# Kernel tuning notes

Hardware: AMD Instinct MI355X
Metric: run time of the kernel (lower is better)

Reference implementation:

```python
import jax, jax.numpy as jnp
import numpy as np

B, T = 32, 64
C, H, W = 1, 32, 32
A, E, D, S, HID = 2, 64, 128, 32, 128
K, STRIDE, PAD = 4, 2, 1
FEAT = 64 * 4 * 4  # conv stack output: 64 channels at 4x4


def _lin(x, w, b):
    return x @ w.T + b


def _conv(x, w, b):
    y = jax.lax.conv_general_dilated(x, w, (STRIDE, STRIDE), [(PAD, PAD)] * 2,
                                     dimension_numbers=('NCHW', 'OIHW', 'NCHW'))
    return y + b[None, :, None, None]


def _deconv(x, w, b):
    # torch ConvTranspose2d(w: (in_c,out_c,k,k), stride=2, pad=1) as dilated conv
    w_ = jnp.flip(w, (2, 3)).transpose(1, 0, 2, 3)
    p = K - 1 - PAD
    y = jax.lax.conv_general_dilated(x, w_, (1, 1), [(p, p)] * 2,
                                     lhs_dilation=(STRIDE, STRIDE),
                                     dimension_numbers=('NCHW', 'OIHW', 'NCHW'))
    return y + b[None, :, None, None]


def _mlp(x, w1, b1, w2, b2, w3, b3):
    h = jax.nn.elu(_lin(x, w1, b1))
    h = jax.nn.elu(_lin(h, w2, b2))
    out = _lin(h, w3, b3)
    return out[..., :S], jnp.clip(out[..., S:], -5.0, 2.0)


def _gru(x, h, wih, whh, bih, bhh):
    # torch nn.GRUCell semantics
    gi = x @ wih.T + bih
    gh = h @ whh.T + bhh
    ir, iz, inn = jnp.split(gi, 3, -1)
    hr, hz, hn = jnp.split(gh, 3, -1)
    r = jax.nn.sigmoid(ir + hr)
    u = jax.nn.sigmoid(iz + hz)
    n = jnp.tanh(inn + r * hn)
    return (1.0 - u) * n + u * h


def setup_inputs():
    keys = iter(jax.random.split(jax.random.key(0), 64))

    def p(shape, fan):
        return jax.random.normal(next(keys), shape, jnp.float32) / np.sqrt(fan)

    return dict(
        obs=jax.random.normal(next(keys), (B, T, C, H, W), jnp.float32),
        actions=jax.random.normal(next(keys), (B, T, A), jnp.float32),
        noise=jax.random.normal(next(keys), (T, B, S), jnp.float32),
        enc_w1=p((32, C, K, K), C * K * K), enc_b1=jnp.zeros(32),
        enc_w2=p((64, 32, K, K), 32 * K * K), enc_b2=jnp.zeros(64),
        enc_w3=p((64, 64, K, K), 64 * K * K), enc_b3=jnp.zeros(64),
        enc_pw=p((E, FEAT), FEAT), enc_pb=jnp.zeros(E),
        dec_pw=p((FEAT, D + S), D + S), dec_pb=jnp.zeros(FEAT),
        dec_w1=p((64, 64, K, K), 64 * K * K), dec_b1=jnp.zeros(64),
        dec_w2=p((64, 32, K, K), 64 * K * K), dec_b2=jnp.zeros(32),
        dec_w3=p((32, C, K, K), 32 * K * K), dec_b3=jnp.zeros(C),
        gru_wih=p((3 * D, S + A), D), gru_whh=p((3 * D, D), D),
        gru_bih=jnp.zeros(3 * D), gru_bhh=jnp.zeros(3 * D),
        pri_w1=p((HID, D + A), D + A), pri_b1=jnp.zeros(HID),
        pri_w2=p((HID, HID), HID), pri_b2=jnp.zeros(HID),
        pri_w3=p((2 * S, HID), HID), pri_b3=jnp.zeros(2 * S),
        pos_w1=p((HID, D + E), D + E), pos_b1=jnp.zeros(HID),
        pos_w2=p((HID, HID), HID), pos_b2=jnp.zeros(HID),
        pos_w3=p((2 * S, HID), HID), pos_b3=jnp.zeros(2 * S),
    )


def reference(obs, actions, noise, enc_w1, enc_b1, enc_w2, enc_b2, enc_w3, enc_b3,
              enc_pw, enc_pb, dec_pw, dec_pb, dec_w1, dec_b1, dec_w2, dec_b2,
              dec_w3, dec_b3, gru_wih, gru_whh, gru_bih, gru_bhh,
              pri_w1, pri_b1, pri_w2, pri_b2, pri_w3, pri_b3,
              pos_w1, pos_b1, pos_w2, pos_b2, pos_w3, pos_b3):
    Bq, Tq = obs.shape[:2]
    # --- CNN encoder over all frames at once ---
    x = obs.reshape(Bq * Tq, C, H, W)
    x = jax.nn.relu(_conv(x, enc_w1, enc_b1))
    x = jax.nn.relu(_conv(x, enc_w2, enc_b2))
    x = jax.nn.relu(_conv(x, enc_w3, enc_b3))
    embed = _lin(x.reshape(Bq * Tq, -1), enc_pw, enc_pb).reshape(Bq, Tq, E)

    # --- sequential RSSM core (use_posterior=True path) ---
    def step(h, inp):
        a, e_t, eps = inp
        pm, pls = _mlp(jnp.concatenate([h, e_t], -1),
                       pos_w1, pos_b1, pos_w2, pos_b2, pos_w3, pos_b3)
        z = pm + jnp.exp(pls) * eps
        prm, prls = _mlp(jnp.concatenate([h, a], -1),
                         pri_w1, pri_b1, pri_w2, pri_b2, pri_w3, pri_b3)
        h_new = _gru(jnp.concatenate([z, a], -1), h, gru_wih, gru_whh, gru_bih, gru_bhh)
        return h_new, (z, prm, prls, pm, pls, h)  # h = pre-update (used for decode)

    h0 = jnp.zeros((Bq, D), obs.dtype)
    h_final, (zs, prm, prls, pm, pls, hs) = jax.lax.scan(
        step, h0, (actions.swapaxes(0, 1), embed.swapaxes(0, 1), noise))

    # --- batched decode of all (h_t, z_t); same math as per-step decode ---
    hz = jnp.concatenate([hs, zs], -1).reshape(Tq * Bq, D + S)
    y = _lin(hz, dec_pw, dec_pb).reshape(Tq * Bq, 64, 4, 4)
    y = jax.nn.relu(_deconv(y, dec_w1, dec_b1))
    y = jax.nn.relu(_deconv(y, dec_w2, dec_b2))
    y = jax.nn.sigmoid(_deconv(y, dec_w3, dec_b3))
    recons = y.reshape(Tq, Bq, C, H, W).swapaxes(0, 1)

    tb = lambda t: t.swapaxes(0, 1)  # (T,B,.) -> (B,T,.)
    return (recons, tb(zs), tb(prm), tb(prls), tb(pm), tb(pls), h_final)
```

## Files before the change

### kernel.cpp

```cpp
#include <hip/hip_runtime.h>
#include <math.h>

#define NB 32
#define NT 64
#define NF 2048

#define OUT_ZS    2097152
#define OUT_PRM   (OUT_ZS + 65536)
#define OUT_PRLS  (OUT_PRM + 65536)
#define OUT_PM    (OUT_PRLS + 65536)
#define OUT_PLS   (OUT_PM + 65536)
#define OUT_HF    (OUT_PLS + 65536)

#define WS_HS    27394048
#define WS_ENCT  27656192
#define WS_WP1H  27885568
#define WS_WP2   27893760
#define WS_WP3   27901952
#define WS_WWHH  27906048
#define WS_WIHZ  27930624
#define WS_PW1T  27977984
#define WS_WIHT  28002560
#define WS_WC2   16777216
#define WS_WC3   (WS_WC2 + 16384)
#define WS_WD1   (WS_WC3 + 32768)
#define WS_WD2   (WS_WD1 + 32768)
#define WS_DLIN  16908288
#define WS_DECWF 17960960
#define WS_QW1F  18045952
#define WS_QW2F  18057216
#define WS_QW3F  18066432
#define WS_POSL1E 25165824
#define WS_GIA    (WS_POSL1E + 262144)

typedef __attribute__((ext_vector_type(8))) short short8;
typedef __attribute__((ext_vector_type(4))) float floatx4;
typedef _Float16 __attribute__((ext_vector_type(2))) half2v;
typedef _Float16 __attribute__((ext_vector_type(8))) half8;
union U4S8 { uint4 u; short8 s; };
__device__ __forceinline__ short8 u2s(uint4 u) { U4S8 x; x.u = u; return x.s; }
union U4HH { uint4 u; half8 h; };
__device__ __forceinline__ half8 u2hh(uint4 u) { U4HH x; x.u = u; return x.h; }

__device__ __forceinline__ float rcpf(float x) {
#if __has_builtin(__builtin_amdgcn_rcpf)
  return __builtin_amdgcn_rcpf(x);
#else
  return 1.f / x;
#endif
}
__device__ __forceinline__ float eluf(float a) {
  return (a > 0.f) ? a : (__expf(a) - 1.f);
}
__device__ __forceinline__ float sigm(float a) {
  return rcpf(1.f + __expf(-a));
}
__device__ __forceinline__ float tanhfast(float x) {
  const float e = __expf(fminf(-2.f * x, 60.f));
  return (1.f - e) * rcpf(1.f + e);
}
__device__ __forceinline__ unsigned short f2bf(float f) {
  unsigned int u = __float_as_uint(f);
  u += 0x7fffu + ((u >> 16) & 1u);
  return (unsigned short)(u >> 16);
}
__device__ __forceinline__ unsigned short f2h(float f) {
  _Float16 h = (_Float16)f;
  return __builtin_bit_cast(unsigned short, h);
}
__device__ __forceinline__ unsigned int pack2h(float a, float b) {
  return (unsigned int)f2h(a) | ((unsigned int)f2h(b) << 16);
}
union UH2 { unsigned int u; half2v h; };
__device__ __forceinline__ half2v u2h(unsigned int u) { UH2 x; x.u = u; return x.h; }

__device__ __forceinline__ float fdot2w(half2v a, half2v b, float c) {
#if __has_builtin(__builtin_amdgcn_fdot2)
  return __builtin_amdgcn_fdot2(a, b, c, false);
#else
  return fmaf((float)a[0], (float)b[0], fmaf((float)a[1], (float)b[1], c));
#endif
}

union U4H2 { uint4 u; half2v h[4]; };
__device__ __forceinline__ void dot8h(uint4 w, uint4 x,
                                      float& a0, float& a1, float& a2, float& a3) {
  U4H2 W; W.u = w;
  U4H2 X; X.u = x;
  a0 = fdot2w(W.h[0], X.h[0], a0);
  a1 = fdot2w(W.h[1], X.h[1], a1);
  a2 = fdot2w(W.h[2], X.h[2], a2);
  a3 = fdot2w(W.h[3], X.h[3], a3);
}

struct PP { const float* src; void* dst; int n; int mode; int A; int B; };
struct PPAll { PP m[16]; };

__global__ __launch_bounds__(256) void k_prep(PPAll a) {
  PP p = a.m[blockIdx.y];
  for (int i = blockIdx.x * 256 + threadIdx.x; i < p.n; i += gridDim.x * 256) {
    if (p.mode == 10) {
      const int r = i / p.B, c = i - r * p.B;
      ((float*)p.dst)[c * p.A + r] = p.src[i];
    } else {
      float v;
      if (p.mode == 0) v = p.src[i];
      else if (p.mode == 1) v = p.src[(i >> 7) * 192 + (i & 127)];
      else if (p.mode == 2) v = p.src[(i >> 5) * 34 + (i & 31)];
      else if (p.mode == 6) {
        const int o = i / 160, k = i - o * 160;
        v = (k < 130) ? p.src[o * 130 + k] : 0.f;
      } else {
        const int ab = p.A * p.B;
        const int t = i / ab, rem = i - t * ab;
        const int oc = rem / p.B, ic = rem - oc * p.B;
        v = (p.mode == 3) ? p.src[(oc * p.B + ic) * 16 + t]
                          : p.src[(ic * p.A + oc) * 16 + t];
      }
      ((unsigned short*)p.dst)[i] = (p.mode <= 2 || p.mode == 6) ? f2h(v) : f2bf(v);
    }
  }
}

__global__ __launch_bounds__(256, 3) void k_enc(
    const float* __restrict__ obs, const float* __restrict__ act,
    const float* __restrict__ w1, const float* __restrict__ b1,
    const unsigned short* __restrict__ wc2, const float* __restrict__ b2,
    const unsigned short* __restrict__ wc3, const float* __restrict__ b3,
    const float* __restrict__ encT, const float* __restrict__ encb,
    const float* __restrict__ pw1T, const float* __restrict__ pb1,
    const float* __restrict__ wihT, const float* __restrict__ bih,
    const float* __restrict__ bhh,
    float* __restrict__ posl1e, float* __restrict__ gia) {
  const int f = blockIdx.x, tid = threadIdx.x;
  const int w = tid >> 6, l = tid & 63, q = l >> 4, n = l & 15;
  __shared__ float sIn1[32 * 33];
  __shared__ float sW1[512];
  __shared__ float sB1[32];
  __shared__ __align__(16) unsigned short sIn2[18 * 18 * 40];
  __shared__ __align__(16) unsigned short sIn3[10 * 10 * 72];
  __shared__ __align__(16) float sXe[1024];
  __shared__ float sP[256];
  __shared__ float sE[64];
  __shared__ float sA2[2];

  {
    const float* in = obs + (size_t)f * 1024;
    for (int i = tid; i < 1024; i += 256) sIn1[(i >> 5) * 33 + (i & 31)] = in[i];
    for (int i = tid; i < 512; i += 256) sW1[i] = w1[i];
    if (tid < 32) sB1[tid] = b1[tid];
    if (tid < 2) sA2[tid] = act[(size_t)f * 2 + tid];
    unsigned int* z2 = (unsigned int*)sIn2;
    for (int i = tid; i < 18 * 18 * 40 / 2; i += 256) z2[i] = 0u;
    unsigned int* z3 = (unsigned int*)sIn3;
    for (int i = tid; i < 10 * 10 * 72 / 2; i += 256) z3[i] = 0u;
  }
  __syncthreads();
  for (int r = tid; r < 512; r += 256) {
    const int oc = r >> 4, oy = r & 15;
    float acc[16];
    const float bv = sB1[oc];
#pragma unroll
    for (int j = 0; j < 16; j++) acc[j] = bv;
#pragma unroll
    for (int ky = 0; ky < 4; ky++) {
      const int iy = 2 * oy + ky - 1;
      if (iy < 0 || iy >= 32) continue;
#pragma unroll
      for (int kx = 0; kx < 4; kx++) {
        const float wv = sW1[oc * 16 + ky * 4 + kx];
#pragma unroll
        for (int j = 0; j < 16; j++) {
          const int ix = 2 * j + kx - 1;
          if (ix >= 0 && ix < 32) acc[j] += wv * sIn1[iy * 33 + ix];
        }
      }
    }
#pragma unroll
    for (int j = 0; j < 16; j++)
      sIn2[((oy + 1) * 18 + (j + 1)) * 40 + oc] = f2bf(fmaxf(acc[j], 0.f));
  }
  __syncthreads();
  {
    int base[4];
#pragma unroll
    for (int nt = 0; nt < 4; nt++) {
      const int px = nt * 16 + n, oy = px >> 3, ox = px & 7;
      base[nt] = ((2 * oy + 1) * 18 + (2 * ox + 1)) * 40 + q * 8;
    }
    floatx4 acc[4];
#pragma unroll
    for (int nt = 0; nt < 4; nt++) acc[nt] = (floatx4){0.f, 0.f, 0.f, 0.f};
    uint4 af[16];
#pragma unroll
    for (int t = 0; t < 16; t++)
      af[t] = *reinterpret_cast<const uint4*>(wc2 + (size_t)(t * 64 + w * 16 + n) * 32 + q * 8);
#pragma unroll
    for (int t = 0; t < 16; t++) {
      const int toff = ((t / 4 - 1) * 18 + (t % 4 - 1)) * 40;
#pragma unroll
      for (int nt = 0; nt < 4; nt++) {
        uint4 bf = *reinterpret_cast<const uint4*>(&sIn2[base[nt] + toff]);
        acc[nt] = __builtin_amdgcn_mfma_f32_16x16x32_bf16(u2s(af[t]), u2s(bf), acc[nt], 0, 0, 0);
      }
    }
    float b4[4];
#pragma unroll
    for (int r = 0; r < 4; r++) b4[r] = b2[w * 16 + q * 4 + r];
    __syncthreads();
#pragma unroll
    for (int nt = 0; nt < 4; nt++) {
      const int px = nt * 16 + n, oy = px >> 3, ox = px & 7;
#pragma unroll
      for (int r = 0; r < 4; r++)
        sIn3[((oy + 1) * 10 + (ox + 1)) * 72 + (w * 16 + q * 4 + r)] =
            f2bf(fmaxf(acc[nt][r] + b4[r], 0.f));
    }
  }
  __syncthreads();
  {
    const int oy = n >> 2, ox = n & 3;
    const int ibase = ((2 * oy + 1) * 10 + (2 * ox + 1)) * 72 + q * 8;
    floatx4 acc = (floatx4){0.f, 0.f, 0.f, 0.f};
    for (int ks = 0; ks < 2; ks++) {
      uint4 af[16];
#pragma unroll
      for (int t = 0; t < 16; t++)
        af[t] = *reinterpret_cast<const uint4*>(
            wc3 + (size_t)(t * 64 + w * 16 + n) * 64 + ks * 32 + q * 8);
#pragma unroll
      for (int t = 0; t < 16; t++) {
        const int toff = ((t / 4 - 1) * 10 + (t % 4 - 1)) * 72 + ks * 32;
        uint4 bf = *reinterpret_cast<const uint4*>(&sIn3[ibase + toff]);
        acc = __builtin_amdgcn_mfma_f32_16x16x32_bf16(u2s(af[t]), u2s(bf), acc, 0, 0, 0);
      }
    }
#pragma unroll
    for (int r = 0; r < 4; r++) {
      const int ch = w * 16 + q * 4 + r;
      sXe[ch * 16 + n] = fmaxf(acc[r] + b3[ch], 0.f);
    }
  }
  __syncthreads();
  {
    const int o = tid & 63, s = tid >> 6;
    float acc = 0.f;
    const int k0 = s * 256;
    for (int k = k0; k < k0 + 256; k++) acc += encT[k * 64 + o] * sXe[k];
    sP[tid] = acc;
  }
  __syncthreads();
  if (tid < 64)
    sE[tid] = sP[tid] + sP[tid + 64] + sP[tid + 128] + sP[tid + 192] + encb[tid];
  __syncthreads();
  if (tid < 128) {
    float a = pb1[tid];
    for (int k = 0; k < 64; k++) a += pw1T[(128 + k) * 128 + tid] * sE[k];
    posl1e[(size_t)f * 128 + tid] = a;
  } else {
#pragma unroll
    for (int jj = 0; jj < 3; jj++) {
      const int j = (tid - 128) + jj * 128;
      gia[(size_t)f * 384 + (tid - 128) * 3 + jj] =
          bih[j] + bhh[j] + wihT[32 * 384 + j] * sA2[0] + wihT[33 * 384 + j] * sA2[1];
    }
  }
}

__global__ __launch_bounds__(512, 2) void k_rssm4(
    const float* __restrict__ posl1e, const float* __restrict__ gia,
    const float* __restrict__ noise,
    const unsigned short* __restrict__ wp1h, const unsigned short* __restrict__ wp2,
    const unsigned short* __restrict__ wp3, const unsigned short* __restrict__ wwhh,
    const unsigned short* __restrict__ wihz,
    const float* __restrict__ pb2, const float* __restrict__ pb3,
    float* __restrict__ hs, float* __restrict__ out) {
  const int b = blockIdx.x, tid = threadIdx.x;
  const int R = tid >> 2, ks4 = tid & 3;
  __shared__ __align__(16) _Float16 sHh[128];
  __shared__ __align__(16) _Float16 sL1h[128];
  __shared__ __align__(16) _Float16 sL2h[128];
  __shared__ __align__(16) _Float16 sZh[32];
  __shared__ float sGh[384];

  uint4 wA4[4][4];
  {
#pragma unroll
    for (int j = 0; j < 4; j++) {
      const unsigned short* p = (j == 0)
          ? (wp1h + R * 128)
          : (wwhh + (size_t)((j - 1) * 128 + R) * 128);
      const uint4* pv = reinterpret_cast<const uint4*>(p + ks4 * 32);
#pragma unroll
      for (int i = 0; i < 4; i++) wA4[j][i] = pv[i];
    }
  }
  uint4 wB[4];
  {
    const unsigned short* rowB = wp2 + R * 128 + ks4 * 32;
#pragma unroll
    for (int i = 0; i < 4; i++) wB[i] = reinterpret_cast<const uint4*>(rowB)[i];
  }
  uint4 wC[2];
  {
    const int r = tid >> 3;
    const int o = (r >> 1) + ((r & 1) << 5);
    const unsigned short* rowC = wp3 + o * 128 + (tid & 7) * 16;
#pragma unroll
    for (int i = 0; i < 2; i++) wC[i] = reinterpret_cast<const uint4*>(rowC)[i];
  }
  uint4 wD[3][4];
  if (tid < 128) {
#pragma unroll
    for (int j = 0; j < 3; j++) {
      const unsigned short* rowD = wihz + (size_t)(tid + 128 * j) * 32;
#pragma unroll
      for (int i = 0; i < 4; i++) wD[j][i] = reinterpret_cast<const uint4*>(rowD)[i];
    }
  }
  const bool zlane = (tid & 15) == 0;
  const int jz = tid >> 4;
  const float pb2R = pb2[R];
  const float pb3mR = zlane ? pb3[jz] : 0.f;
  const float pb3sR = zlane ? pb3[jz + 32] : 0.f;

  float h_reg = 0.f;
  float pl1R = 0.f, epsR = 0.f;
  float3 gaR = {0.f, 0.f, 0.f};
  if (ks4 == 0) pl1R = posl1e[(size_t)(b * 64) * 128 + R];
  if (tid < 128) {
    gaR = *reinterpret_cast<const float3*>(&gia[(size_t)(b * 64) * 384 + tid * 3]);
    sHh[tid] = (_Float16)0.f;
    hs[(size_t)b * 128 + tid] = 0.f;
  }
  if (zlane) epsR = noise[(size_t)b * 32 + jz];
  __syncthreads();

  for (int t = 0; t < 64; ++t) {
    const int tn = (t < 63) ? t + 1 : 63;
    float pl1N = 0.f, epsN = 0.f;
    float3 gaN = {0.f, 0.f, 0.f};
    if (ks4 == 0) pl1N = posl1e[(size_t)(b * 64 + tn) * 128 + R];
    if (tid < 128)
      gaN = *reinterpret_cast<const float3*>(&gia[(size_t)(b * 64 + tn) * 384 + tid * 3]);
    if (zlane) epsN = noise[(size_t)(tn * 32 + b) * 32 + jz];

    {
      const uint4* xs = reinterpret_cast<const uint4*>(sHh) + ks4 * 4;
      const uint4 x0 = xs[0], x1 = xs[1], x2 = xs[2], x3 = xs[3];
      float part[4];
#pragma unroll
      for (int j = 0; j < 4; j++) {
        float p0 = 0.f, p1 = 0.f, p2 = 0.f, p3 = 0.f;
        dot8h(wA4[j][0], x0, p0, p1, p2, p3);
        dot8h(wA4[j][1], x1, p0, p1, p2, p3);
        dot8h(wA4[j][2], x2, p0, p1, p2, p3);
        dot8h(wA4[j][3], x3, p0, p1, p2, p3);
        part[j] = (p0 + p1) + (p2 + p3);
      }
#pragma unroll
      for (int j = 0; j < 4; j++) {
        part[j] += __shfl_xor(part[j], 1);
        part[j] += __shfl_xor(part[j], 2);
      }
      if (ks4 == 0) {
        sL1h[R] = (_Float16)eluf(part[0] + pl1R);
        sGh[R * 3] = part[1];
        sGh[R * 3 + 1] = part[2];
        sGh[R * 3 + 2] = part[3];
      }
    }
    __syncthreads();
    {
      float a0 = 0.f, a1 = 0.f, a2 = 0.f, a3 = 0.f;
      const uint4* xs = reinterpret_cast<const uint4*>(sL1h) + ks4 * 4;
#pragma unroll
      for (int i = 0; i < 4; i++) dot8h(wB[i], xs[i], a0, a1, a2, a3);
      float p = (a0 + a1) + (a2 + a3);
      p += __shfl_xor(p, 1);
      p += __shfl_xor(p, 2);
      if (ks4 == 0) sL2h[R] = (_Float16)eluf(p + pb2R);
    }
    __syncthreads();
    {
      float a0 = 0.f, a1 = 0.f, a2 = 0.f, a3 = 0.f;
      const uint4* xs = reinterpret_cast<const uint4*>(sL2h) + (tid & 7) * 2;
      dot8h(wC[0], xs[0], a0, a1, a2, a3);
      dot8h(wC[1], xs[1], a0, a1, a2, a3);
      float p = (a0 + a1) + (a2 + a3);
      p += __shfl_xor(p, 1);
      p += __shfl_xor(p, 2);
      p += __shfl_xor(p, 4);
      const float pq = __shfl_xor(p, 8);
      if (zlane) {
        const float pm = p + pb3mR;
        float pls = pq + pb3sR;
        pls = fminf(fmaxf(pls, -5.f), 2.f);
        const float z = pm + __expf(pls) * epsR;
        sZh[jz] = (_Float16)z;
        const int o = (b * 64 + t) * 32 + jz;
        out[OUT_ZS + o] = z;
        out[OUT_PM + o] = pm;
        out[OUT_PLS + o] = pls;
      }
    }
    __syncthreads();
    if (tid < 128) {
      float r0 = 0.f, r1 = 0.f, r2 = 0.f, r3 = 0.f;
      float u0 = 0.f, u1 = 0.f, u2 = 0.f, u3 = 0.f;
      float m0 = 0.f, m1 = 0.f, m2 = 0.f, m3 = 0.f;
      const uint4* xs = reinterpret_cast<const uint4*>(sZh);
#pragma unroll
      for (int i = 0; i < 4; i++) {
        const uint4 xv = xs[i];
        dot8h(wD[0][i], xv, r0, r1, r2, r3);
        dot8h(wD[1][i], xv, u0, u1, u2, u3);
        dot8h(wD[2][i], xv, m0, m1, m2, m3);
      }
      const float gr = gaR.x + ((r0 + r1) + (r2 + r3));
      const float gu = gaR.y + ((u0 + u1) + (u2 + u3));
      const float gn = gaR.z + ((m0 + m1) + (m2 + m3));
      const float ghr = sGh[tid * 3];
      const float ghu = sGh[tid * 3 + 1];
      const float ghn = sGh[tid * 3 + 2];
      const float r = sigm(gr + ghr);
      const float u = sigm(gu + ghu);
      const float n = tanhfast(gn + r * ghn);
      const float hn = (1.f - u) * n + u * h_reg;
      h_reg = hn;
      sHh[tid] = (_Float16)hn;
      if (t < 63) hs[(size_t)((t + 1) * 32 + b) * 128 + tid] = hn;
    }
    pl1R = pl1N;
    gaR = gaN;
    epsR = epsN;
    __syncthreads();
  }
  if (tid < 128) out[OUT_HF + b * 128 + tid] = h_reg;
}

__global__ __launch_bounds__(256) void k_post(
    const float* __restrict__ hs, const float* __restrict__ zs,
    const unsigned short* __restrict__ decwf, const float* __restrict__ decb,
    unsigned short* __restrict__ dlin,
    const float* __restrict__ act,
    const unsigned short* __restrict__ qw1f, const float* __restrict__ qb1,
    const unsigned short* __restrict__ qw2f, const float* __restrict__ qb2,
    const unsigned short* __restrict__ qw3f, const float* __restrict__ qb3,
    float* __restrict__ out) {
  const int tid = threadIdx.x;
  const int bid = blockIdx.x;
  const int w = tid >> 6, l = tid & 63, q = l >> 4, n = l & 15;
  __shared__ __align__(16) _Float16 sB[16][168];
  __shared__ __align__(16) _Float16 sB2[16][136];

  if (bid < 2048) {
    const int otile = bid & 15;
    const int fBase = (bid >> 4) * 16;
    for (int i = tid; i < 2560; i += 256) {
      const int fr = i / 160, k = i - fr * 160;
      const int f = fBase + fr;
      float v;
      if (k < 128) v = hs[(size_t)f * 128 + k];
      else v = zs[(size_t)((f & 31) * 64 + (f >> 5)) * 32 + (k - 128)];
      sB[fr][k] = (_Float16)v;
    }
    __syncthreads();
    const int oB = otile * 64 + w * 16;
    floatx4 acc = (floatx4){0.f, 0.f, 0.f, 0.f};
#pragma unroll
    for (int ks = 0; ks < 5; ks++) {
      uint4 a = *reinterpret_cast<const uint4*>(&decwf[(size_t)(oB + n) * 160 + ks * 32 + q * 8]);
      uint4 bb = *reinterpret_cast<const uint4*>(&sB[n][ks * 32 + q * 8]);
      acc = __builtin_amdgcn_mfma_f32_16x16x32_f16(u2hh(a), u2hh(bb), acc, 0, 0, 0);
    }
    const int o0 = oB + q * 4;
    const int f = fBase + n;
    const unsigned int lo = (unsigned int)f2bf(acc[0] + decb[o0]) |
                            ((unsigned int)f2bf(acc[1] + decb[o0 + 1]) << 16);
    const unsigned int hi = (unsigned int)f2bf(acc[2] + decb[o0 + 2]) |
                            ((unsigned int)f2bf(acc[3] + decb[o0 + 3]) << 16);
    *reinterpret_cast<uint2*>(&dlin[(size_t)f * 1024 + o0]) = make_uint2(lo, hi);
    return;
  }
  const int fBase = (bid - 2048) * 16;
  for (int i = tid; i < 2560; i += 256) {
    const int fr = i / 160, k = i - fr * 160;
    const int f = fBase + fr;
    float v = 0.f;
    if (k < 128) v = hs[(size_t)f * 128 + k];
    else if (k < 130) v = act[(size_t)((f & 31) * 64 + (f >> 5)) * 2 + (k - 128)];
    sB[fr][k] = (_Float16)v;
  }
  __syncthreads();
#pragma unroll
  for (int g = 0; g < 2; g++) {
    const int oB = g * 64 + w * 16;
    floatx4 acc = (floatx4){0.f, 0.f, 0.f, 0.f};
#pragma unroll
    for (int ks = 0; ks < 5; ks++) {
      uint4 a = *reinterpret_cast<const uint4*>(&qw1f[(oB + n) * 160 + ks * 32 + q * 8]);
      uint4 bb = *reinterpret_cast<const uint4*>(&sB[n][ks * 32 + q * 8]);
      acc = __builtin_amdgcn_mfma_f32_16x16x32_f16(u2hh(a), u2hh(bb), acc, 0, 0, 0);
    }
    const int o0 = oB + q * 4;
    *reinterpret_cast<unsigned int*>(&sB2[n][o0]) =
        pack2h(eluf(acc[0] + qb1[o0]), eluf(acc[1] + qb1[o0 + 1]));
    *reinterpret_cast<unsigned int*>(&sB2[n][o0 + 2]) =
        pack2h(eluf(acc[2] + qb1[o0 + 2]), eluf(acc[3] + qb1[o0 + 3]));
  }
  __syncthreads();
#pragma unroll
  for (int g = 0; g < 2; g++) {
    const int oB = g * 64 + w * 16;
    floatx4 acc = (floatx4){0.f, 0.f, 0.f, 0.f};
#pragma unroll
    for (int ks = 0; ks < 4; ks++) {
      uint4 a = *reinterpret_cast<const uint4*>(&qw2f[(oB + n) * 128 + ks * 32 + q * 8]);
      uint4 bb = *reinterpret_cast<const uint4*>(&sB2[n][ks * 32 + q * 8]);
      acc = __builtin_amdgcn_mfma_f32_16x16x32_f16(u2hh(a), u2hh(bb), acc, 0, 0, 0);
    }
    const int o0 = oB + q * 4;
    *reinterpret_cast<unsigned int*>(&sB[n][o0]) =
        pack2h(eluf(acc[0] + qb2[o0]), eluf(acc[1] + qb2[o0 + 1]));
    *reinterpret_cast<unsigned int*>(&sB[n][o0 + 2]) =
        pack2h(eluf(acc[2] + qb2[o0 + 2]), eluf(acc[3] + qb2[o0 + 3]));
  }
  __syncthreads();
  {
    const int oB = w * 16;
    floatx4 acc = (floatx4){0.f, 0.f, 0.f, 0.f};
#pragma unroll
    for (int ks = 0; ks < 4; ks++) {
      uint4 a = *reinterpret_cast<const uint4*>(&qw3f[(oB + n) * 128 + ks * 32 + q * 8]);
      uint4 bb = *reinterpret_cast<const uint4*>(&sB[n][ks * 32 + q * 8]);
      acc = __builtin_amdgcn_mfma_f32_16x16x32_f16(u2hh(a), u2hh(bb), acc, 0, 0, 0);
    }
    const int o0 = oB + q * 4;
    const int f = fBase + n;
    const int ob = ((f & 31) * 64 + (f >> 5)) * 32;
#pragma unroll
    for (int r = 0; r < 4; r++) {
      const int o = o0 + r;
      const float v = acc[r] + qb3[o];
      if (o < 32) out[OUT_PRM + ob + o] = v;
      else out[OUT_PRLS + ob + o - 32] = fminf(fmaxf(v, -5.f), 2.f);
    }
  }
}

#define D3_ROW 580
#define D3_PX  36
__global__ __launch_bounds__(256, 4) void k_dec(
    const unsigned short* __restrict__ dlin,
    const unsigned short* __restrict__ wd1, const float* __restrict__ db1,
    const unsigned short* __restrict__ wd2, const float* __restrict__ db2,
    const float* __restrict__ w3, const float* __restrict__ b3,
    float* __restrict__ out) {
  const int f = blockIdx.x, tid = threadIdx.x;
  const int w = tid >> 6, l = tid & 63, q = l >> 4, n = l & 15;
  const int t = f >> 5, b = f & 31;
  __shared__ __align__(16) unsigned short sInD1[6 * 6 * 72];
  __shared__ __align__(16) unsigned short sInD2[10 * 10 * 72];
  __shared__ __align__(16) _Float16 sInD3h[16 * D3_ROW];
  __shared__ __align__(16) _Float16 sW3h[16 * 32];

  const uint2 dv = *reinterpret_cast<const uint2*>(dlin + (size_t)f * 1024 + tid * 4);
  {
    unsigned int* z1 = (unsigned int*)sInD1;
    for (int i = tid; i < 6 * 6 * 72 / 2; i += 256) z1[i] = 0u;
    unsigned int* z2 = (unsigned int*)sInD2;
    for (int i = tid; i < 10 * 10 * 72 / 2; i += 256) z2[i] = 0u;
    for (int s = tid; s < 512; s += 256) {
      const int tap = s >> 5, icc = s & 31;
      sW3h[s] = (_Float16)w3[icc * 16 + tap];
    }
  }
  __syncthreads();
  {
    const int o0 = tid * 4, c = o0 >> 4, px0 = o0 & 15;
    const int Y = px0 >> 2;
    const int base = ((Y + 1) * 6 + 1) * 72 + c;
    sInD1[base] = (unsigned short)(dv.x & 0xffffu);
    sInD1[base + 72] = (unsigned short)(dv.x >> 16);
    sInD1[base + 144] = (unsigned short)(dv.y & 0xffffu);
    sInD1[base + 216] = (unsigned short)(dv.y >> 16);
  }
  __syncthreads();
  {
    const int Y = n >> 2, X = n & 3;
    const int ibase = ((Y + 1) * 6 + (X + 1)) * 72 + q * 8;
    float b4[4];
#pragma unroll
    for (int r = 0; r < 4; r++) b4[r] = db1[w * 16 + q * 4 + r];
#pragma unroll
    for (int c = 0; c < 4; c++) {
      const int cy = c >> 1, cx = c & 1;
      floatx4 acc = (floatx4){0.f, 0.f, 0.f, 0.f};
      for (int ks = 0; ks < 2; ks++) {
        uint4 af[4];
#pragma unroll
        for (int tt = 0; tt < 4; tt++) {
          const int t2 = tt >> 1, t3 = tt & 1;
          const int ky = ((cy + 1) & 1) + 2 * t2, kx = ((cx + 1) & 1) + 2 * t3;
          af[tt] = *reinterpret_cast<const uint4*>(
              wd1 + (size_t)((ky * 4 + kx) * 64 + w * 16 + n) * 64 + ks * 32 + q * 8);
        }
#pragma unroll
        for (int tt = 0; tt < 4; tt++) {
          const int t2 = tt >> 1, t3 = tt & 1;
          const int toff = ((cy - t2) * 6 + (cx - t3)) * 72 + ks * 32;
          uint4 bf = *reinterpret_cast<const uint4*>(&sInD1[ibase + toff]);
          acc = __builtin_amdgcn_mfma_f32_16x16x32_bf16(u2s(af[tt]), u2s(bf), acc, 0, 0, 0);
        }
      }
      const int oy = 2 * Y + cy, ox = 2 * X + cx;
#pragma unroll
      for (int r = 0; r < 4; r++)
        sInD2[((oy + 1) * 10 + (ox + 1)) * 72 + (w * 16 + q * 4 + r)] =
            f2bf(fmaxf(acc[r] + b4[r], 0.f));
    }
  }
  __syncthreads();
  {
    const int px = w * 16 + n;
    const int Y = px >> 3, X = px & 7;
    const int ibase = ((Y + 1) * 10 + (X + 1)) * 72 + q * 8;
    float b4[2][4];
#pragma unroll
    for (int mi = 0; mi < 2; mi++)
#pragma unroll
      for (int r = 0; r < 4; r++) b4[mi][r] = db2[mi * 16 + q * 4 + r];
#pragma unroll
    for (int c = 0; c < 4; c++) {
      const int cy = c >> 1, cx = c & 1;
      floatx4 acc[2];
      acc[0] = (floatx4){0.f, 0.f, 0.f, 0.f};
      acc[1] = (floatx4){0.f, 0.f, 0.f, 0.f};
      for (int ks = 0; ks < 2; ks++) {
        uint4 af[2][4];
#pragma unroll
        for (int mi = 0; mi < 2; mi++)
#pragma unroll
          for (int tt = 0; tt < 4; tt++) {
            const int t2 = tt >> 1, t3 = tt & 1;
            const int ky = ((cy + 1) & 1) + 2 * t2, kx = ((cx + 1) & 1) + 2 * t3;
            af[mi][tt] = *reinterpret_cast<const uint4*>(
                wd2 + (size_t)((ky * 4 + kx) * 32 + mi * 16 + n) * 64 + ks * 32 + q * 8);
          }
#pragma unroll
        for (int tt = 0; tt < 4; tt++) {
          const int t2 = tt >> 1, t3 = tt & 1;
          const int toff = ((cy - t2) * 10 + (cx - t3)) * 72 + ks * 32;
          uint4 bf = *reinterpret_cast<const uint4*>(&sInD2[ibase + toff]);
#pragma unroll
          for (int mi = 0; mi < 2; mi++)
            acc[mi] = __builtin_amdgcn_mfma_f32_16x16x32_bf16(u2s(af[mi][tt]), u2s(bf),
                                                              acc[mi], 0, 0, 0);
        }
      }
      const int oy = 2 * Y + cy, ox = 2 * X + cx;
#pragma unroll
      for (int mi = 0; mi < 2; mi++) {
        const unsigned int lo =
            (unsigned int)f2h(fmaxf(acc[mi][0] + b4[mi][0], 0.f)) |
            ((unsigned int)f2h(fmaxf(acc[mi][1] + b4[mi][1], 0.f)) << 16);
        const unsigned int hi =
            (unsigned int)f2h(fmaxf(acc[mi][2] + b4[mi][2], 0.f)) |
            ((unsigned int)f2h(fmaxf(acc[mi][3] + b4[mi][3], 0.f)) << 16);
        *reinterpret_cast<uint2*>(&sInD3h[oy * D3_ROW + ox * D3_PX + mi * 16 + q * 4]) =
            make_uint2(lo, hi);
      }
    }
  }
  __syncthreads();
  {
    const int oy = tid >> 3;
    const int rem2 = tid & 7;
    const int cpar = rem2 >> 2, qq = rem2 & 3;
    const int py = (oy + 1) & 1, pc = (cpar + 1) & 1;
    const int ixb0 = (cpar + 1 - pc) >> 1;
    const int xlo = ixb0 - 1 + qq * 4;
    float acc[4] = {0.f, 0.f, 0.f, 0.f};
    const float bv = b3[0];
#pragma unroll
    for (int u2 = 0; u2 < 2; u2++) {
      const int ky = py + 2 * u2;
      const int iy = (oy + 1 - ky) >> 1;
      if (iy < 0 || iy >= 16) continue;
      const _Float16* rowp = &sInD3h[iy * D3_ROW];
      const uint2* wAp = reinterpret_cast<const uint2*>(&sW3h[(ky * 4 + pc) * 32]);
      const uint2* wBp = reinterpret_cast<const uint2*>(&sW3h[(ky * 4 + pc + 2) * 32]);
#pragma unroll
      for (int kb = 0; kb < 8; kb++) {
        uint2 xv[5];
#pragma unroll
        for (int x = 0; x < 5; x++) {
          const int ix = xlo + x;
          xv[x] = (ix >= 0 && ix < 16)
              ? *reinterpret_cast<const uint2*>(&rowp[ix * D3_PX + kb * 4])
              : make_uint2(0u, 0u);
        }
        const uint2 wa = wAp[kb], wb = wBp[kb];
#pragma unroll
        for (int j = 0; j < 4; j++) {
          acc[j] = fdot2w(u2h(wa.x), u2h(xv[j + 1].x), acc[j]);
          acc[j] = fdot2w(u2h(wa.y), u2h(xv[j + 1].y), acc[j]);
          acc[j] = fdot2w(u2h(wb.x), u2h(xv[j].x), acc[j]);
          acc[j] = fdot2w(u2h(wb.y), u2h(xv[j].y), acc[j]);
        }
      }
    }
    const int fo = b * 64 + t;
    float* yf = out + (size_t)fo * 1024;
#pragma unroll
    for (int j = 0; j < 4; j++)
      yf[oy * 32 + (cpar + 2 * (qq * 4 + j))] = rcpf(1.f + __expf(-(acc[j] + bv)));
  }
}

extern "C" void kernel_launch(void* const* d_in, const int* in_sizes, int n_in,
                              void* d_out, int out_size, void* d_ws, size_t ws_size,
                              hipStream_t stream) {
  const float* obs = (const float*)d_in[0];
  const float* actions = (const float*)d_in[1];
  const float* noise = (const float*)d_in[2];
  const float* enc_w1 = (const float*)d_in[3];
  const float* enc_b1 = (const float*)d_in[4];
  const float* enc_w2 = (const float*)d_in[5];
  const float* enc_b2 = (const float*)d_in[6];
  const float* enc_w3 = (const float*)d_in[7];
  const float* enc_b3 = (const float*)d_in[8];
  const float* enc_pw = (const float*)d_in[9];
  const float* enc_pb = (const float*)d_in[10];
  const float* dec_pw = (const float*)d_in[11];
  const float* dec_pb = (const float*)d_in[12];
  const float* dec_w1 = (const float*)d_in[13];
  const float* dec_b1 = (const float*)d_in[14];
  const float* dec_w2 = (const float*)d_in[15];
  const float* dec_b2 = (const float*)d_in[16];
  const float* dec_w3 = (const float*)d_in[17];
  const float* dec_b3 = (const float*)d_in[18];
  const float* gru_wih = (const float*)d_in[19];
  const float* gru_whh = (const float*)d_in[20];
  const float* gru_bih = (const float*)d_in[21];
  const float* gru_bhh = (const float*)d_in[22];
  const float* pri_w1 = (const float*)d_in[23];
  const float* pri_b1 = (const float*)d_in[24];
  const float* pri_w2 = (const float*)d_in[25];
  const float* pri_b2 = (const float*)d_in[26];
  const float* pri_w3 = (const float*)d_in[27];
  const float* pri_b3 = (const float*)d_in[28];
  const float* pos_w1 = (const float*)d_in[29];
  const float* pos_b1 = (const float*)d_in[30];
  const float* pos_w2 = (const float*)d_in[31];
  const float* pos_b2 = (const float*)d_in[32];
  const float* pos_w3 = (const float*)d_in[33];
  const float* pos_b3 = (const float*)d_in[34];

  float* out = (float*)d_out;
  float* ws = (float*)d_ws;
  float* HS = ws + WS_HS;
  float* POSL1E = ws + WS_POSL1E;
  float* GIA = ws + WS_GIA;
  unsigned short* WP1H = (unsigned short*)(ws + WS_WP1H);
  unsigned short* WP2 = (unsigned short*)(ws + WS_WP2);
  unsigned short* WP3 = (unsigned short*)(ws + WS_WP3);
  unsigned short* WWHH = (unsigned short*)(ws + WS_WWHH);
  unsigned short* WIHZ = (unsigned short*)(ws + WS_WIHZ);
  unsigned short* WC2 = (unsigned short*)(ws + WS_WC2);
  unsigned short* WC3 = (unsigned short*)(ws + WS_WC3);
  unsigned short* WD1 = (unsigned short*)(ws + WS_WD1);
  unsigned short* WD2 = (unsigned short*)(ws + WS_WD2);
  unsigned short* DLIN = (unsigned short*)(ws + WS_DLIN);
  unsigned short* DECWF = (unsigned short*)(ws + WS_DECWF);
  unsigned short* QW1F = (unsigned short*)(ws + WS_QW1F);
  unsigned short* QW2F = (unsigned short*)(ws + WS_QW2F);
  unsigned short* QW3F = (unsigned short*)(ws + WS_QW3F);

  PPAll pp;
  pp.m[0]  = {enc_pw, ws + WS_ENCT, 64 * 1024, 10, 64, 1024};
  pp.m[1]  = {dec_pw, DECWF, 1024 * 160, 0, 0, 0};
  pp.m[2]  = {pri_w1, QW1F, 128 * 160, 6, 0, 0};
  pp.m[3]  = {pri_w2, QW2F, 128 * 128, 0, 0, 0};
  pp.m[4]  = {pri_w3, QW3F, 64 * 128, 0, 0, 0};
  pp.m[5]  = {pos_w1, ws + WS_PW1T, 128 * 192, 10, 128, 192};
  pp.m[6]  = {gru_wih, ws + WS_WIHT, 384 * 34, 10, 384, 34};
  pp.m[7]  = {pos_w1, WP1H, 128 * 128, 1, 0, 0};
  pp.m[8]  = {pos_w2, WP2, 128 * 128, 0, 0, 0};
  pp.m[9]  = {pos_w3, WP3, 64 * 128, 0, 0, 0};
  pp.m[10] = {gru_whh, WWHH, 384 * 128, 0, 0, 0};
  pp.m[11] = {gru_wih, WIHZ, 384 * 32, 2, 0, 0};
  pp.m[12] = {enc_w2, WC2, 16 * 64 * 32, 3, 64, 32};
  pp.m[13] = {enc_w3, WC3, 16 * 64 * 64, 3, 64, 64};
  pp.m[14] = {dec_w1, WD1, 16 * 64 * 64, 4, 64, 64};
  pp.m[15] = {dec_w2, WD2, 16 * 32 * 64, 4, 32, 64};
  hipLaunchKernelGGL(k_prep, dim3(32, 16), dim3(256), 0, stream, pp);

  k_enc<<<NF, 256, 0, stream>>>(obs, actions, enc_w1, enc_b1, WC2, enc_b2,
                                WC3, enc_b3, ws + WS_ENCT, enc_pb,
                                ws + WS_PW1T, pos_b1, ws + WS_WIHT, gru_bih,
                                gru_bhh, POSL1E, GIA);

  k_rssm4<<<NB, 512, 0, stream>>>(POSL1E, GIA, noise, WP1H, WP2, WP3, WWHH, WIHZ,
                                  pos_b2, pos_b3, HS, out);

  k_post<<<2176, 256, 0, stream>>>(HS, out + OUT_ZS, DECWF, dec_pb, DLIN,
                                   actions, QW1F, pri_b1, QW2F, pri_b2,
                                   QW3F, pri_b3, out);

  k_dec<<<NF, 256, 0, stream>>>(DLIN, WD1, dec_b1, WD2, dec_b2, dec_w3, dec_b3, out);
}
```

Before: 437.8 us.

## Move encoder projection and posterior layer-1 embed term to batched MFMA kernel

The per-frame scalar GEMV for the encoder projection (1024->64) and the posterior first-layer embedding contribution are removed from k_enc. k_enc now writes fp16 conv features to workspace, and a new k_emb kernel processes 16 frames per block with f16 MFMA, using fp16 copies of the weights prepared in k_prep. The aim is to replace slow per-frame fp32 dot products with tensor-core GEMMs that reuse the weights across frames. The cost is an extra launch and a global round trip for the features, plus reduced precision from fp16 rounding of the features and the embedding.

```diff
diff --git a/kernel.cpp b/kernel.cpp
--- a/kernel.cpp
+++ b/kernel.cpp
@@ -13,13 +13,13 @@
 #define OUT_HF    (OUT_PLS + 65536)
 
 #define WS_HS    27394048
-#define WS_ENCT  27656192
+#define WS_ENCWF 27656192
 #define WS_WP1H  27885568
 #define WS_WP2   27893760
 #define WS_WP3   27901952
 #define WS_WWHH  27906048
 #define WS_WIHZ  27930624
-#define WS_PW1T  27977984
+#define WS_PW1E  27977984
 #define WS_WIHT  28002560
 #define WS_WC2   16777216
 #define WS_WC3   (WS_WC2 + 16384)
@@ -30,6 +30,7 @@
 #define WS_QW1F  18045952
 #define WS_QW2F  18057216
 #define WS_QW3F  18066432
+#define WS_XE    18874368
 #define WS_POSL1E 25165824
 #define WS_GIA    (WS_POSL1E + 262144)
 
@@ -110,6 +111,8 @@
       else if (p.mode == 6) {
         const int o = i / 160, k = i - o * 160;
         v = (k < 130) ? p.src[o * 130 + k] : 0.f;
+      } else if (p.mode == 7) {
+        v = p.src[(i >> 6) * 192 + 128 + (i & 63)];
       } else {
         const int ab = p.A * p.B;
         const int t = i / ab, rem = i - t * ab;
@@ -117,7 +120,7 @@
         v = (p.mode == 3) ? p.src[(oc * p.B + ic) * 16 + t]
                           : p.src[(ic * p.A + oc) * 16 + t];
       }
-      ((unsigned short*)p.dst)[i] = (p.mode <= 2 || p.mode == 6) ? f2h(v) : f2bf(v);
+      ((unsigned short*)p.dst)[i] = (p.mode <= 2 || p.mode >= 6) ? f2h(v) : f2bf(v);
     }
   }
 }
@@ -127,11 +130,9 @@
     const float* __restrict__ w1, const float* __restrict__ b1,
     const unsigned short* __restrict__ wc2, const float* __restrict__ b2,
     const unsigned short* __restrict__ wc3, const float* __restrict__ b3,
-    const float* __restrict__ encT, const float* __restrict__ encb,
-    const float* __restrict__ pw1T, const float* __restrict__ pb1,
     const float* __restrict__ wihT, const float* __restrict__ bih,
     const float* __restrict__ bhh,
-    float* __restrict__ posl1e, float* __restrict__ gia) {
+    unsigned short* __restrict__ xe, float* __restrict__ gia) {
   const int f = blockIdx.x, tid = threadIdx.x;
   const int w = tid >> 6, l = tid & 63, q = l >> 4, n = l & 15;
   __shared__ float sIn1[32 * 33];
@@ -139,9 +140,7 @@
   __shared__ float sB1[32];
   __shared__ __align__(16) unsigned short sIn2[18 * 18 * 40];
   __shared__ __align__(16) unsigned short sIn3[10 * 10 * 72];
-  __shared__ __align__(16) float sXe[1024];
-  __shared__ float sP[256];
-  __shared__ float sE[64];
+  __shared__ __align__(16) _Float16 sXeh[1024];
   __shared__ float sA2[2];
 
   {
@@ -238,32 +237,71 @@
 #pragma unroll
     for (int r = 0; r < 4; r++) {
       const int ch = w * 16 + q * 4 + r;
-      sXe[ch * 16 + n] = fmaxf(acc[r] + b3[ch], 0.f);
-    }
-  }
-  __syncthreads();
-  {
-    const int o = tid & 63, s = tid >> 6;
-    float acc = 0.f;
-    const int k0 = s * 256;
-    for (int k = k0; k < k0 + 256; k++) acc += encT[k * 64 + o] * sXe[k];
-    sP[tid] = acc;
-  }
-  __syncthreads();
-  if (tid < 64)
-    sE[tid] = sP[tid] + sP[tid + 64] + sP[tid + 128] + sP[tid + 192] + encb[tid];
-  __syncthreads();
-  if (tid < 128) {
-    float a = pb1[tid];
-    for (int k = 0; k < 64; k++) a += pw1T[(128 + k) * 128 + tid] * sE[k];
-    posl1e[(size_t)f * 128 + tid] = a;
-  } else {
+      sXeh[ch * 16 + n] = (_Float16)fmaxf(acc[r] + b3[ch], 0.f);
+    }
+  }
+  __syncthreads();
+  *reinterpret_cast<uint2*>(&xe[(size_t)f * 1024 + tid * 4]) =
+      *reinterpret_cast<const uint2*>(&sXeh[tid * 4]);
+  if (tid >= 128) {
 #pragma unroll
     for (int jj = 0; jj < 3; jj++) {
       const int j = (tid - 128) + jj * 128;
       gia[(size_t)f * 384 + (tid - 128) * 3 + jj] =
           bih[j] + bhh[j] + wihT[32 * 384 + j] * sA2[0] + wihT[33 * 384 + j] * sA2[1];
     }
+  }
+}
+
+__global__ __launch_bounds__(256) void k_emb(
+    const unsigned short* __restrict__ xe,
+    const unsigned short* __restrict__ encwf, const float* __restrict__ encb,
+    const unsigned short* __restrict__ pw1e, const float* __restrict__ pb1,
+    float* __restrict__ posl1e) {
+  const int tid = threadIdx.x;
+  const int fBase = blockIdx.x * 16;
+  const int w = tid >> 6, l = tid & 63, q = l >> 4, n = l & 15;
+  __shared__ __align__(16) _Float16 sB[16][1032];
+  __shared__ __align__(16) _Float16 sE2[16][72];
+#pragma unroll
+  for (int j = 0; j < 8; j++) {
+    const int i4 = tid + j * 256;
+    const int fr = i4 >> 7, kq = (i4 & 127) * 8;
+    *reinterpret_cast<uint4*>(&sB[fr][kq]) =
+        *reinterpret_cast<const uint4*>(&xe[(size_t)(fBase + fr) * 1024 + kq]);
+  }
+  __syncthreads();
+  {
+    const int oB = w * 16;
+    floatx4 acc = (floatx4){0.f, 0.f, 0.f, 0.f};
+#pragma unroll
+    for (int ks = 0; ks < 32; ks++) {
+      uint4 a = *reinterpret_cast<const uint4*>(
+          &encwf[(size_t)(oB + n) * 1024 + ks * 32 + q * 8]);
+      uint4 bb = *reinterpret_cast<const uint4*>(&sB[n][ks * 32 + q * 8]);
+      acc = __builtin_amdgcn_mfma_f32_16x16x32_f16(u2hh(a), u2hh(bb), acc, 0, 0, 0);
+    }
+    const int o0 = oB + q * 4;
+    *reinterpret_cast<unsigned int*>(&sE2[n][o0]) =
+        pack2h(acc[0] + encb[o0], acc[1] + encb[o0 + 1]);
+    *reinterpret_cast<unsigned int*>(&sE2[n][o0 + 2]) =
+        pack2h(acc[2] + encb[o0 + 2], acc[3] + encb[o0 + 3]);
+  }
+  __syncthreads();
+#pragma unroll
+  for (int g = 0; g < 2; g++) {
+    const int oB = g * 64 + w * 16;
+    floatx4 acc = (floatx4){0.f, 0.f, 0.f, 0.f};
+#pragma unroll
+    for (int ks = 0; ks < 2; ks++) {
+      uint4 a = *reinterpret_cast<const uint4*>(&pw1e[(oB + n) * 64 + ks * 32 + q * 8]);
+      uint4 bb = *reinterpret_cast<const uint4*>(&sE2[n][ks * 32 + q * 8]);
+      acc = __builtin_amdgcn_mfma_f32_16x16x32_f16(u2hh(a), u2hh(bb), acc, 0, 0, 0);
+    }
+    const int o0 = oB + q * 4;
+#pragma unroll
+    for (int r = 0; r < 4; r++)
+      posl1e[(size_t)(fBase + n) * 128 + o0 + r] = acc[r] + pb1[o0 + r];
   }
 }
 
@@ -777,14 +815,17 @@
   unsigned short* QW1F = (unsigned short*)(ws + WS_QW1F);
   unsigned short* QW2F = (unsigned short*)(ws + WS_QW2F);
   unsigned short* QW3F = (unsigned short*)(ws + WS_QW3F);
+  unsigned short* ENCWF = (unsigned short*)(ws + WS_ENCWF);
+  unsigned short* PW1E = (unsigned short*)(ws + WS_PW1E);
+  unsigned short* XE = (unsigned short*)(ws + WS_XE);
 
   PPAll pp;
-  pp.m[0]  = {enc_pw, ws + WS_ENCT, 64 * 1024, 10, 64, 1024};
+  pp.m[0]  = {enc_pw, ENCWF, 64 * 1024, 0, 0, 0};
   pp.m[1]  = {dec_pw, DECWF, 1024 * 160, 0, 0, 0};
   pp.m[2]  = {pri_w1, QW1F, 128 * 160, 6, 0, 0};
   pp.m[3]  = {pri_w2, QW2F, 128 * 128, 0, 0, 0};
   pp.m[4]  = {pri_w3, QW3F, 64 * 128, 0, 0, 0};
-  pp.m[5]  = {pos_w1, ws + WS_PW1T, 128 * 192, 10, 128, 192};
+  pp.m[5]  = {pos_w1, PW1E, 128 * 64, 7, 0, 0};
   pp.m[6]  = {gru_wih, ws + WS_WIHT, 384 * 34, 10, 384, 34};
   pp.m[7]  = {pos_w1, WP1H, 128 * 128, 1, 0, 0};
   pp.m[8]  = {pos_w2, WP2, 128 * 128, 0, 0, 0};
@@ -798,9 +839,10 @@
   hipLaunchKernelGGL(k_prep, dim3(32, 16), dim3(256), 0, stream, pp);
 
   k_enc<<<NF, 256, 0, stream>>>(obs, actions, enc_w1, enc_b1, WC2, enc_b2,
-                                WC3, enc_b3, ws + WS_ENCT, enc_pb,
-                                ws + WS_PW1T, pos_b1, ws + WS_WIHT, gru_bih,
-                                gru_bhh, POSL1E, GIA);
+                                WC3, enc_b3, ws + WS_WIHT, gru_bih, gru_bhh,
+                                XE, GIA);
+
+  k_emb<<<128, 256, 0, stream>>>(XE, ENCWF, enc_pb, PW1E, pos_b1, POSL1E);
 
   k_rssm4<<<NB, 512, 0, stream>>>(POSL1E, GIA, noise, WP1H, WP2, WP3, WWHH, WIHZ,
                                   pos_b2, pos_b3, HS, out);
```

New measurement: 434.5 us, median of 2. Within noise of the previous version (-0.8%).
